# Kernel tuning notes

Hardware: AMD Instinct MI355X
Metric: run time of the kernel (lower is better)

## Reference

```python
import jax, jax.numpy as jnp
import numpy as np

SIZE = 48          # grid edge
DIST = 4           # local neighborhood edge
PAD = DIST // 2    # padding = 2
PADDED = SIZE + 2 * PAD  # 52
RATE = 5           # recurrent steps
CONVEY = 0.9
N_IN = 2048        # input injection sites


def setup_inputs() -> dict:
    key = jax.random.key(0)
    ks = jax.random.split(key, 8)
    neuron_matrix = jnp.zeros((PADDED, PADDED, PADDED), dtype=jnp.float32)
    vinput = jax.random.normal(ks[0], (N_IN,), dtype=jnp.float32)
    # scale synapse so the 5-step relu recurrence stays numerically tame
    synapse = jax.random.normal(ks[1], (SIZE, SIZE, SIZE, DIST, DIST, DIST), dtype=jnp.float32) * 0.05
    W1 = jax.random.normal(ks[2], (SIZE ** 3, 1024), dtype=jnp.float32) * (1.0 / np.sqrt(SIZE ** 3))
    b1 = jnp.zeros((1024,), dtype=jnp.float32)
    W2 = jax.random.normal(ks[3], (1024, 128), dtype=jnp.float32) * (1.0 / np.sqrt(1024))
    b2 = jnp.zeros((128,), dtype=jnp.float32)
    W3 = jax.random.normal(ks[4], (128, 10), dtype=jnp.float32) * (1.0 / np.sqrt(128))
    b3 = jnp.zeros((10,), dtype=jnp.float32)
    node_idx = jax.random.randint(ks[5], (N_IN, 3), 0, SIZE)  # interior coords
    return {"neuron_matrix": neuron_matrix, "vinput": vinput, "synapse": synapse,
            "W1": W1, "b1": b1, "W2": W2, "b2": b2, "W3": W3, "b3": b3,
            "node_idx": node_idx}


def _windows(p):
    # p: [PADDED]^3 -> sliding DxDxD windows at every interior site: [S,S,S,D,D,D]
    idx = jnp.arange(SIZE)[:, None] + jnp.arange(DIST)[None, :]  # [S, D]
    w = jnp.take(p, idx, axis=0)   # [S, D, P, P]
    w = jnp.take(w, idx, axis=2)   # [S, D, S, D, P]
    w = jnp.take(w, idx, axis=4)   # [S, D, S, D, S, D]
    return jnp.transpose(w, (0, 2, 4, 1, 3, 5))  # [S, S, S, D, D, D]


def reference(neuron_matrix, vinput, synapse, W1, b1, W2, b2, W3, b3, node_idx):
    # inject inputs at (possibly colliding) interior nodes (scatter-add, like +=)
    nm = neuron_matrix.at[node_idx[:, 0] + PAD,
                          node_idx[:, 1] + PAD,
                          node_idx[:, 2] + PAD].add(vinput)
    # recurrent locally-connected 3D neighbor aggregation, RATE steps
    for _ in range(RATE):
        win = _windows(nm)  # [S,S,S,D,D,D]
        agg = jnp.einsum('xyzabc,xyzabc->xyz', synapse, win)  # per-site unique-weight reduce
        interior = jax.nn.relu(agg) * CONVEY
        nm = jnp.pad(interior, PAD)  # re-pad with zeros for next step
    x = interior.reshape(1, SIZE ** 3)
    x = jax.nn.relu(x @ W1 + b1)
    x = jax.nn.relu(x @ W2 + b2)
    return x @ W3 + b3  # [1, 10]
```

## Files before the change

### kernel.cpp

```cpp
#include <hip/hip_runtime.h>

#define S 48
#define D 4
#define PADC 2
#define P 52
#define SITES (S * S * S)
#define PADVOL (P * P * P)
#define N_IN 2048
#define H1 1024
#define H2 128
#define OUTN 10
#define RP 64
#define NCH (SITES / RP)
#define RG 16
#define CHPG (NCH / RG)
#define G2B 32

__global__ __launch_bounds__(256) void zero_k(float4* __restrict__ p, int n4,
                                              int* __restrict__ cnt) {
    int i = blockIdx.x * 256 + threadIdx.x;
    if (i < n4) p[i] = make_float4(0.f, 0.f, 0.f, 0.f);
    if (i == 0) *cnt = 0;
}

__global__ void scatter_k(const float* __restrict__ vin,
                          const int* __restrict__ idx,
                          float* __restrict__ nm) {
    int t = blockIdx.x * blockDim.x + threadIdx.x;
    if (t < N_IN) {
        int x = idx[t * 3 + 0] + PADC;
        int y = idx[t * 3 + 1] + PADC;
        int z = idx[t * 3 + 2] + PADC;
        atomicAdd(&nm[(x * P + y) * P + z], vin[t]);
    }
}

__global__ __launch_bounds__(256) void step_k(const float* __restrict__ src,
                                              const float* __restrict__ syn,
                                              float* __restrict__ dst) {
    int tid = threadIdx.x;
    int q = tid & 3;
    int sl = tid >> 2;
    int s = blockIdx.x * 64 + sl;
    int z = s % S;
    int t2 = s / S;
    int y = t2 % S;
    int x = t2 / S;
    const float4* sv = (const float4*)(syn + (size_t)s * 64);
    float acc = 0.0f;
#pragma unroll
    for (int a = 0; a < D; a++) {
        const float* row = src + ((x + a) * P + (y + q)) * P + z;
        float4 w = sv[a * 4 + q];
        acc += w.x * row[0] + w.y * row[1] + w.z * row[2] + w.w * row[3];
    }
    acc += __shfl_xor(acc, 1);
    acc += __shfl_xor(acc, 2);
    if (q == 0) {
        dst[((x + PADC) * P + (y + PADC)) * P + (z + PADC)] = fmaxf(acc, 0.0f) * 0.9f;
    }
}

__global__ __launch_bounds__(256) void gemv1f_k(const float* __restrict__ src,
                                                const float* __restrict__ syn,
                                                const float* __restrict__ W1,
                                                float* __restrict__ partial) {
    int t = threadIdx.x;
    int lane = t & 63;
    int i0 = blockIdx.x * RP;

    int s = i0 + lane;
    int z = s % S;
    int q = s / S;
    int y = q % S;
    int x = q / S;
    const float4* sv = (const float4*)(syn + (size_t)s * 64);
    float sum = 0.0f;
#pragma unroll
    for (int a = 0; a < D; a++) {
#pragma unroll
        for (int b = 0; b < D; b++) {
            const float* row = src + ((x + a) * P + (y + b)) * P + z;
            float4 w = sv[a * 4 + b];
            sum += w.x * row[0] + w.y * row[1] + w.z * row[2] + w.w * row[3];
        }
    }
    float v = fmaxf(sum, 0.0f) * 0.9f;
    unsigned long long mask = __ballot(v != 0.0f);

    const float4* W4 = (const float4*)W1;
    size_t base = (size_t)i0 * (H1 / 4) + t;
    float4 a0 = {0.f, 0.f, 0.f, 0.f};
    float4 a1 = {0.f, 0.f, 0.f, 0.f};
    float4 a2 = {0.f, 0.f, 0.f, 0.f};
    float4 a3 = {0.f, 0.f, 0.f, 0.f};
    int nnz = __popcll(mask);
    for (int k = 0; k + 4 <= nnz; k += 4) {
        int r0 = (int)__builtin_ctzll(mask); mask &= mask - 1;
        int r1 = (int)__builtin_ctzll(mask); mask &= mask - 1;
        int r2 = (int)__builtin_ctzll(mask); mask &= mask - 1;
        int r3 = (int)__builtin_ctzll(mask); mask &= mask - 1;
        float x0 = __int_as_float(__builtin_amdgcn_readlane(__float_as_int(v), r0));
        float x1 = __int_as_float(__builtin_amdgcn_readlane(__float_as_int(v), r1));
        float x2 = __int_as_float(__builtin_amdgcn_readlane(__float_as_int(v), r2));
        float x3 = __int_as_float(__builtin_amdgcn_readlane(__float_as_int(v), r3));
        float4 w0 = W4[base + (size_t)r0 * (H1 / 4)];
        float4 w1 = W4[base + (size_t)r1 * (H1 / 4)];
        float4 w2 = W4[base + (size_t)r2 * (H1 / 4)];
        float4 w3 = W4[base + (size_t)r3 * (H1 / 4)];
        a0.x += x0 * w0.x; a0.y += x0 * w0.y; a0.z += x0 * w0.z; a0.w += x0 * w0.w;
        a1.x += x1 * w1.x; a1.y += x1 * w1.y; a1.z += x1 * w1.z; a1.w += x1 * w1.w;
        a2.x += x2 * w2.x; a2.y += x2 * w2.y; a2.z += x2 * w2.z; a2.w += x2 * w2.w;
        a3.x += x3 * w3.x; a3.y += x3 * w3.y; a3.z += x3 * w3.z; a3.w += x3 * w3.w;
    }
    while (mask) {
        int r0 = (int)__builtin_ctzll(mask); mask &= mask - 1;
        float x0 = __int_as_float(__builtin_amdgcn_readlane(__float_as_int(v), r0));
        float4 w0 = W4[base + (size_t)r0 * (H1 / 4)];
        a0.x += x0 * w0.x; a0.y += x0 * w0.y; a0.z += x0 * w0.z; a0.w += x0 * w0.w;
    }
    float4 acc = {a0.x + a1.x + a2.x + a3.x,
                  a0.y + a1.y + a2.y + a3.y,
                  a0.z + a1.z + a2.z + a3.z,
                  a0.w + a1.w + a2.w + a3.w};
    ((float4*)(partial + (size_t)blockIdx.x * H1))[t] = acc;
}

__global__ __launch_bounds__(256) void reduceA_k(const float* __restrict__ partial,
                                                 float* __restrict__ redB) {
    int g = blockIdx.x >> 2;
    int c = (blockIdx.x & 3) * 256 + threadIdx.x;
    float s = 0.0f;
    int r0 = g * CHPG;
#pragma unroll 4
    for (int r = r0; r < r0 + CHPG; r++) s += partial[(size_t)r * H1 + c];
    redB[g * H1 + c] = s;
}

__global__ __launch_bounds__(128) void gemv2f_k(const float* __restrict__ redB,
                                                const float* __restrict__ b1,
                                                const float* __restrict__ W2,
                                                const float* __restrict__ b2,
                                                const float* __restrict__ W3,
                                                const float* __restrict__ b3,
                                                float* __restrict__ partial2,
                                                int* __restrict__ cnt,
                                                float* __restrict__ out) {
    __shared__ float ys[H1 / G2B];
    __shared__ int amlast;
    int b = blockIdx.x;
    int t = threadIdx.x;
    int r0 = b * (H1 / G2B);
    if (t < H1 / G2B) {
        int j = r0 + t;
        float s = b1[j];
#pragma unroll
        for (int g = 0; g < RG; g++) s += redB[g * H1 + j];
        ys[t] = fmaxf(s, 0.0f);
    }
    __syncthreads();
    float acc = 0.0f;
#pragma unroll
    for (int i = 0; i < H1 / G2B; i++)
        acc += ys[i] * W2[(size_t)(r0 + i) * H2 + t];
    partial2[b * H2 + t] = acc;

    __threadfence();
    __syncthreads();
    if (t == 0) {
        int prev = atomicAdd(cnt, 1);
        amlast = (prev == G2B - 1) ? 1 : 0;
    }
    __syncthreads();
    if (amlast) {
        __threadfence();
        __shared__ float y2[H2];
        float s2 = b2[t];
#pragma unroll
        for (int k = 0; k < G2B; k++) s2 += partial2[k * H2 + t];
        y2[t] = fmaxf(s2, 0.0f);
        __syncthreads();
        if (t < OUTN) {
            float o = b3[t];
#pragma unroll 8
            for (int k = 0; k < H2; k++) o += y2[k] * W3[k * OUTN + t];
            out[t] = o;
        }
    }
}

extern "C" void kernel_launch(void* const* d_in, const int* in_sizes, int n_in,
                              void* d_out, int out_size, void* d_ws, size_t ws_size,
                              hipStream_t stream) {
    const float* vinput  = (const float*)d_in[1];
    const float* synapse = (const float*)d_in[2];
    const float* W1      = (const float*)d_in[3];
    const float* b1      = (const float*)d_in[4];
    const float* W2      = (const float*)d_in[5];
    const float* b2      = (const float*)d_in[6];
    const float* W3      = (const float*)d_in[7];
    const float* b3      = (const float*)d_in[8];
    const int* node_idx  = (const int*)d_in[9];

    float* ws = (float*)d_ws;
    float* nm0 = ws;
    float* nm1 = nm0 + PADVOL;
    float* partial1 = nm1 + PADVOL;
    float* redB = partial1 + (size_t)NCH * H1;
    float* partial2 = redB + RG * H1;
    int* cnt = (int*)(partial2 + G2B * H2);
    float* out = (float*)d_out;

    const int n4 = 2 * PADVOL / 4;
    zero_k<<<(n4 + 255) / 256, 256, 0, stream>>>((float4*)nm0, n4, cnt);

    scatter_k<<<N_IN / 256, 256, 0, stream>>>(vinput, node_idx, nm0);

    const float* src = nm0;
    float* dst = nm1;
    for (int r = 0; r < 4; r++) {
        step_k<<<SITES / 64, 256, 0, stream>>>(src, synapse, dst);
        float* tmp = (float*)src;
        src = dst;
        dst = tmp;
    }

    gemv1f_k<<<NCH, 256, 0, stream>>>(src, synapse, W1, partial1);
    reduceA_k<<<RG * 4, 256, 0, stream>>>(partial1, redB);
    gemv2f_k<<<G2B, 128, 0, stream>>>(redB, b1, W2, b2, W3, b3,
                                      partial2, cnt, out);
}
```

Before: 99.81 us.

## Prefetch W1 into cache during recurrent steps and unfuse final step from GEMV

```diff
diff --git a/kernel.cpp b/kernel.cpp
--- a/kernel.cpp
+++ b/kernel.cpp
@@ -15,6 +15,7 @@
 #define RG 16
 #define CHPG (NCH / RG)
 #define G2B 32
+#define WARM4 884736
 
 __global__ __launch_bounds__(256) void zero_k(float4* __restrict__ p, int n4,
                                               int* __restrict__ cnt) {
@@ -37,7 +38,9 @@
 
 __global__ __launch_bounds__(256) void step_k(const float* __restrict__ src,
                                               const float* __restrict__ syn,
-                                              float* __restrict__ dst) {
+                                              float* __restrict__ dst,
+                                              const float4* __restrict__ w1warm,
+                                              int step) {
     int tid = threadIdx.x;
     int q = tid & 3;
     int sl = tid >> 2;
@@ -47,6 +50,11 @@
     int y = t2 % S;
     int x = t2 / S;
     const float4* sv = (const float4*)(syn + (size_t)s * 64);
+
+    size_t gt = (size_t)blockIdx.x * 256 + tid;
+    float4 wm0 = w1warm[(size_t)step * WARM4 + gt * 2];
+    float4 wm1 = w1warm[(size_t)step * WARM4 + gt * 2 + 1];
+
     float acc = 0.0f;
 #pragma unroll
     for (int a = 0; a < D; a++) {
@@ -59,33 +67,23 @@
     if (q == 0) {
         dst[((x + PADC) * P + (y + PADC)) * P + (z + PADC)] = fmaxf(acc, 0.0f) * 0.9f;
     }
-}
-
-__global__ __launch_bounds__(256) void gemv1f_k(const float* __restrict__ src,
-                                                const float* __restrict__ syn,
-                                                const float* __restrict__ W1,
-                                                float* __restrict__ partial) {
+    asm volatile("" :: "v"(wm0.x), "v"(wm0.y), "v"(wm0.z), "v"(wm0.w),
+                       "v"(wm1.x), "v"(wm1.y), "v"(wm1.z), "v"(wm1.w));
+}
+
+__global__ __launch_bounds__(256) void gemv1_k(const float* __restrict__ nmfin,
+                                               const float* __restrict__ W1,
+                                               float* __restrict__ partial) {
     int t = threadIdx.x;
     int lane = t & 63;
     int i0 = blockIdx.x * RP;
 
-    int s = i0 + lane;
-    int z = s % S;
-    int q = s / S;
+    int i = i0 + lane;
+    int z = i % S;
+    int q = i / S;
     int y = q % S;
     int x = q / S;
-    const float4* sv = (const float4*)(syn + (size_t)s * 64);
-    float sum = 0.0f;
-#pragma unroll
-    for (int a = 0; a < D; a++) {
-#pragma unroll
-        for (int b = 0; b < D; b++) {
-            const float* row = src + ((x + a) * P + (y + b)) * P + z;
-            float4 w = sv[a * 4 + b];
-            sum += w.x * row[0] + w.y * row[1] + w.z * row[2] + w.w * row[3];
-        }
-    }
-    float v = fmaxf(sum, 0.0f) * 0.9f;
+    float v = nmfin[((x + PADC) * P + (y + PADC)) * P + (z + PADC)];
     unsigned long long mask = __ballot(v != 0.0f);
 
     const float4* W4 = (const float4*)W1;
@@ -218,14 +216,15 @@
 
     const float* src = nm0;
     float* dst = nm1;
-    for (int r = 0; r < 4; r++) {
-        step_k<<<SITES / 64, 256, 0, stream>>>(src, synapse, dst);
+    for (int r = 0; r < 5; r++) {
+        step_k<<<SITES / 64, 256, 0, stream>>>(src, synapse, dst,
+                                               (const float4*)W1, r);
         float* tmp = (float*)src;
         src = dst;
         dst = tmp;
     }
 
-    gemv1f_k<<<NCH, 256, 0, stream>>>(src, synapse, W1, partial1);
+    gemv1_k<<<NCH, 256, 0, stream>>>(nm1, W1, partial1);
     reduceA_k<<<RG * 4, 256, 0, stream>>>(partial1, redB);
     gemv2f_k<<<G2B, 128, 0, stream>>>(redB, b1, W2, b2, W3, b3,
                                       partial2, cnt, out);
```

Result: slower. 110.5 us (+10.7%).
